# Optimization experiments

Measured on AMD Instinct MI355X. Metric: run time of the kernel, lower is better.

## Reference

```python
import jax, jax.numpy as jnp
import numpy as np

# AF2 IPA dims
N, CS, CZ, E, PQ, PV, H = 768, 384, 128, 16, 4, 8, 12
SCALE_SINGLE = 1.0 / np.sqrt(E)
SCALE_FRAME = -1.0 / np.sqrt(18.0 * PQ)


def setup_inputs() -> dict:
    key = jax.random.key(0)
    ks = jax.random.split(key, 14)
    single = jax.random.normal(ks[0], (N, CS), jnp.float32)
    pair = jax.random.normal(ks[1], (N, N, CZ), jnp.float32)
    R, _ = jnp.linalg.qr(jax.random.normal(ks[2], (N, 3, 3), jnp.float32))  # proper per-residue rotations
    t = jax.random.normal(ks[3], (N, 3), jnp.float32)

    def w(k, shape):
        return jax.random.normal(k, shape, jnp.float32) / np.sqrt(shape[0])

    Wq = w(ks[4], (CS, H * E))
    Wk = w(ks[5], (CS, H * E))
    Wv = w(ks[6], (CS, H * E))
    Wqp = w(ks[7], (CS, H * PQ * 3))
    Wkp = w(ks[8], (CS, H * PQ * 3))
    Wvp = w(ks[9], (CS, H * PV * 3))
    Wb = w(ks[10], (CZ, H))
    D_out = H * (CZ + E + PV * 4)  # 2112
    Wout = w(ks[11], (D_out, CS))
    bout = jnp.zeros((CS,), jnp.float32)
    scale_head = jnp.ones((H,), jnp.float32)
    return dict(single_representation=single, pair_representation=pair,
                frame_rotations=R, frame_translations=t,
                Wq=Wq, Wk=Wk, Wv=Wv, Wqp=Wqp, Wkp=Wkp, Wvp=Wvp,
                Wb=Wb, Wout=Wout, bout=bout, scale_head=scale_head)


def reference(single_representation, pair_representation, frame_rotations, frame_translations,
              Wq, Wk, Wv, Wqp, Wkp, Wvp, Wb, Wout, bout, scale_head):
    s, z, R, t = single_representation, pair_representation, frame_rotations, frame_translations
    # --- attention weights from three sources ---
    q = (s @ Wq).reshape(N, H, E)
    k = (s @ Wk).reshape(N, H, E)
    v = (s @ Wv).reshape(N, H, E)
    w_single = SCALE_SINGLE * jnp.einsum('ihe,jhe->hij', q, k)  # [H,N,N]
    w_pair = (z @ Wb).transpose(2, 0, 1)                        # [H,N,N]

    qp = (s @ Wqp).reshape(N, H, PQ, 3)
    kp = (s @ Wkp).reshape(N, H, PQ, 3)
    # Frame.apply: x_global = R_n x + t_n
    gq = jnp.einsum('nab,nhpb->nhpa', R, qp) + t[:, None, None, :]
    gk = jnp.einsum('nab,nhpb->nhpa', R, kp) + t[:, None, None, :]
    # sum_p ||gq_i^hp - gk_j^hp||^2 expanded to avoid [N,N,H,P,3] intermediate
    sq_q = jnp.sum(gq * gq, axis=(-1, -2)).T   # [H,N]
    sq_k = jnp.sum(gk * gk, axis=(-1, -2)).T   # [H,N]
    dot = jnp.einsum('ihpc,jhpc->hij', gq, gk)
    d2 = sq_q[:, :, None] + sq_k[:, None, :] - 2.0 * dot  # [H,N,N]
    w_frame = SCALE_FRAME * jax.nn.softplus(scale_head)[:, None, None] * d2

    a = jax.nn.softmax(w_single + w_pair + w_frame, axis=-1)  # [H,N,N]

    # --- three value paths ---
    o_s = jnp.einsum('hij,jhe->ihe', a, v).reshape(N, H * E)
    o_z = jnp.einsum('hij,ijc->ihc', a, z).reshape(N, H * CZ)

    vp = (s @ Wvp).reshape(N, H, PV, 3)
    gv = jnp.einsum('nab,nhpb->nhpa', R, vp) + t[:, None, None, :]
    so = jnp.einsum('hij,jhpc->ihpc', a, gv)                    # [N,H,PV,3] in global frame
    # Frame.inverse applied: R_i^T (x - t_i)
    local = jnp.einsum('nba,nhpb->nhpa', R, so - t[:, None, None, :])
    pts = local.transpose(0, 2, 1, 3).reshape(N, PV * H * 3)    # (point, head, xyz) flatten
    norms = jnp.linalg.norm(local, axis=-1).transpose(0, 2, 1).reshape(N, PV * H)

    att = jnp.concatenate([o_s, o_z, pts, norms], axis=-1)      # [N, H*(E+CZ+4*PV)]
    return att @ Wout + bout
```

## Files before the change

### kernel.cpp

```cpp
#include <hip/hip_runtime.h>
#include <hip/hip_bf16.h>

#define NN 768
#define CSD 384
#define CZD 128
#define HD 12
#define DOUT 2112
#define II 2

#define SCALE_SINGLE 0.25f
#define SCALE_FRAME (-0.11785113019775793f)

__device__ __forceinline__ float dot4f(float4 a, float4 b){
    return fmaf(a.x,b.x, fmaf(a.y,b.y, fmaf(a.z,b.z, a.w*b.w)));
}

__global__ __launch_bounds__(384) void k_proj(
    const float* __restrict__ s, const float* __restrict__ R, const float* __restrict__ tv,
    const float* __restrict__ Wq, const float* __restrict__ Wk, const float* __restrict__ Wv,
    const float* __restrict__ Wqp, const float* __restrict__ Wkp, const float* __restrict__ Wvp,
    float* __restrict__ q, float* __restrict__ k, float* __restrict__ v,
    float* __restrict__ gq, float* __restrict__ gk, float* __restrict__ gv,
    float* __restrict__ sqq, float* __restrict__ sqk)
{
    __shared__ float s_l[II*CSD];
    __shared__ float praw[II][576];
    __shared__ float sq_pt[II][96];
    int i0 = blockIdx.x * II, t = threadIdx.x;
    if (t < II*CSD/4){
        const float4* s4 = (const float4*)(s + (size_t)i0*CSD);
        ((float4*)s_l)[t] = s4[t];
    }
    __syncthreads();

    int cols[3] = {t, t+384, t+768};
    const float* Wp[3]; int st[3], lc[3];
    #pragma unroll
    for (int m=0;m<3;m++){
        int c = cols[m];
        if (c < 192){ Wp[m]=Wq;  st[m]=192; lc[m]=c; }
        else if (c < 384){ Wp[m]=Wk;  st[m]=192; lc[m]=c-192; }
        else if (c < 576){ Wp[m]=Wv;  st[m]=192; lc[m]=c-384; }
        else if (c < 720){ Wp[m]=Wqp; st[m]=144; lc[m]=c-576; }
        else if (c < 864){ Wp[m]=Wkp; st[m]=144; lc[m]=c-720; }
        else { Wp[m]=Wvp; st[m]=288; lc[m]=c-864; }
    }
    float acc[3][II];
    #pragma unroll
    for (int m=0;m<3;m++)
        #pragma unroll
        for (int ii=0;ii<II;ii++) acc[m][ii]=0.f;

    #pragma unroll 4
    for (int r=0;r<CSD;r++){
        float w0 = Wp[0][(size_t)r*st[0]+lc[0]];
        float w1 = Wp[1][(size_t)r*st[1]+lc[1]];
        float w2 = Wp[2][(size_t)r*st[2]+lc[2]];
        #pragma unroll
        for (int ii=0;ii<II;ii++){
            float sv = s_l[ii*CSD + r];
            acc[0][ii] = fmaf(sv, w0, acc[0][ii]);
            acc[1][ii] = fmaf(sv, w1, acc[1][ii]);
            acc[2][ii] = fmaf(sv, w2, acc[2][ii]);
        }
    }
    #pragma unroll
    for (int m=0;m<3;m++){
        int c = cols[m];
        #pragma unroll
        for (int ii=0;ii<II;ii++){
            float val = acc[m][ii];
            size_t i = i0 + ii;
            if (c < 192) q[i*192 + c] = val;
            else if (c < 384) k[i*192 + (c-192)] = val;
            else if (c < 576) v[i*192 + (c-384)] = val;
            else praw[ii][c-576] = val;
        }
    }
    __syncthreads();

    if (t < 192){
        #pragma unroll
        for (int ii=0;ii<II;ii++){
            size_t i = i0 + ii;
            const float* Ri = R + i*9;
            float R00=Ri[0],R01=Ri[1],R02=Ri[2];
            float R10=Ri[3],R11=Ri[4],R12=Ri[5];
            float R20=Ri[6],R21=Ri[7],R22=Ri[8];
            float t0=tv[i*3+0],t1=tv[i*3+1],t2=tv[i*3+2];
            int src; float* dst; int sqslot=-1;
            if (t < 48){ src = t*3; dst = gq + i*144 + t*3; sqslot = t; }
            else if (t < 96){ int u=t-48; src = 144+u*3; dst = gk + i*144 + u*3; sqslot = 48+u; }
            else { int u=t-96; src = 288+u*3; dst = gv + i*288 + u*3; }
            float x=praw[ii][src], y=praw[ii][src+1], zc=praw[ii][src+2];
            float g0 = fmaf(R00,x, fmaf(R01,y, fmaf(R02,zc, t0)));
            float g1 = fmaf(R10,x, fmaf(R11,y, fmaf(R12,zc, t1)));
            float g2 = fmaf(R20,x, fmaf(R21,y, fmaf(R22,zc, t2)));
            dst[0]=g0; dst[1]=g1; dst[2]=g2;
            if (sqslot >= 0) sq_pt[ii][sqslot] = g0*g0 + g1*g1 + g2*g2;
        }
    }
    __syncthreads();
    if (t < II*HD){
        int ii = t / HD, h = t % HD;
        float s1 = sq_pt[ii][h*4]+sq_pt[ii][h*4+1]+sq_pt[ii][h*4+2]+sq_pt[ii][h*4+3];
        float s2 = sq_pt[ii][48+h*4]+sq_pt[ii][48+h*4+1]+sq_pt[ii][48+h*4+2]+sq_pt[ii][48+h*4+3];
        sqq[(size_t)(i0+ii)*HD + h] = s1;
        sqk[(size_t)(i0+ii)*HD + h] = s2;
    }
}

__global__ __launch_bounds__(512) void k_ipa(
    const float* __restrict__ z, const float* __restrict__ Wb, const float* __restrict__ scale_head,
    const float* __restrict__ q, const float* __restrict__ k,
    const float* __restrict__ gq, const float* __restrict__ gk,
    const float* __restrict__ sqq, const float* __restrict__ sqk,
    const float* __restrict__ v, const float* __restrict__ gv,
    const float* __restrict__ R, const float* __restrict__ tv,
    float* __restrict__ att)
{
    __shared__ float ztile[2][64][CZD];
    __shared__ float wbT[HD*CZD];
    __shared__ float qloc[360];
    __shared__ float a_l[HD][NN];
    __shared__ float so_l[288];

    int i = blockIdx.x, t = threadIdx.x;
    int wave = t >> 6, lane = t & 63;

    for (int idx=t; idx<HD*CZD; idx+=512){
        int h = idx >> 7, c = idx & 127;
        wbT[idx] = Wb[(size_t)c*HD + h];
    }
    if (t < 192) qloc[t] = q[(size_t)i*192 + t];
    else if (t < 336) qloc[t] = gq[(size_t)i*144 + (t-192)];
    else if (t < 348) qloc[t] = sqq[(size_t)i*HD + (t-336)];
    else if (t < 360){
        int h = t-348;
        float shv = scale_head[h];
        float sp = (shv > 20.f) ? shv : log1pf(__expf(shv));
        qloc[t] = SCALE_FRAME * sp;
    }

    const char* zi = (const char*)(z + (size_t)i*NN*CZD);
    float* zbase = &ztile[0][0][0];

#define STAGEL(JT, BUF) do { \
    const char* _zb = zi + (size_t)(JT)*32768; \
    char* _lb = (char*)zbase + (size_t)(BUF)*32768; \
    _Pragma("unroll") \
    for (int _m=0;_m<4;_m++){ \
        int _d = t*16 + _m*8192; \
        int _j = _d >> 9; \
        int _b = _d & 511; \
        int _sb = _b ^ ((_j & 31) << 4); \
        __builtin_amdgcn_global_load_lds((const __attribute__((address_space(1))) void*)(_zb + (size_t)_j*512 + _sb), \
            (__attribute__((address_space(3))) void*)(_lb + _d), 16, 0, 0); \
    } \
  } while(0)

#define STAGEB(JT, BUF) do { \
    const float* _s = (const float*)zi + (size_t)(JT)*4096 + t*4; \
    float* _d = zbase + (size_t)(BUF)*4096 + t*4; \
    __builtin_amdgcn_global_load_lds((const __attribute__((address_space(1))) void*)_s, \
        (__attribute__((address_space(3))) void*)_d, 16, 0, 0); \
    __builtin_amdgcn_global_load_lds((const __attribute__((address_space(1))) void*)(_s+2048), \
        (__attribute__((address_space(3))) void*)(_d+2048), 16, 0, 0); \
  } while(0)

    STAGEL(0, 0);

    int hg = (wave < 4) ? wave : (wave - 4);
    int h0 = hg * 3;
    float L[12][3];

    __syncthreads();

    {
        const float4* wb4 = (const float4*)wbT;
        const float4* qv4 = (const float4*)qloc;
        const float4* gq4 = (const float4*)(qloc + 192);
        int xoff = (lane & 31) << 4;

        for (int jt=0; jt<12; ++jt){
            int cur = jt & 1;
            if (jt+1 < 12) STAGEL(jt+1, cur^1);
            if (wave < 4){
                const char* zb = (const char*)(zbase + (size_t)cur*8192) + lane*512;
                float p0=0.f, p1=0.f, p2=0.f;
                #pragma unroll 8
                for (int c4=0; c4<32; ++c4){
                    float4 zv = *(const float4*)(zb + ((c4*16) ^ xoff));
                    p0 += dot4f(zv, wb4[(h0+0)*32 + c4]);
                    p1 += dot4f(zv, wb4[(h0+1)*32 + c4]);
                    p2 += dot4f(zv, wb4[(h0+2)*32 + c4]);
                }
                L[jt][0]=p0; L[jt][1]=p1; L[jt][2]=p2;
            } else {
                int jg = jt*64 + lane;
                const float4* kp  = (const float4*)(k  + (size_t)jg*192);
                const float4* gkp = (const float4*)(gk + (size_t)jg*144);
                #pragma unroll
                for (int hs=0; hs<3; ++hs){
                    int h = h0 + hs;
                    float sng = dot4f(qv4[h*4+0], kp[h*4+0]) + dot4f(qv4[h*4+1], kp[h*4+1])
                              + dot4f(qv4[h*4+2], kp[h*4+2]) + dot4f(qv4[h*4+3], kp[h*4+3]);
                    float fdot = dot4f(gq4[h*3+0], gkp[h*3+0]) + dot4f(gq4[h*3+1], gkp[h*3+1])
                               + dot4f(gq4[h*3+2], gkp[h*3+2]);
                    float d2 = qloc[336+h] + sqk[(size_t)jg*HD + h] - 2.0f*fdot;
                    L[jt][hs] = fmaf(SCALE_SINGLE, sng, qloc[348+h]*d2);
                }
            }
            __syncthreads();
        }
    }

    float* S_l = zbase;
    if (wave >= 4){
        int base = (hg*64 + lane) * 37;
        #pragma unroll
        for (int jt=0; jt<12; ++jt)
            #pragma unroll
            for (int hs=0; hs<3; ++hs)
                S_l[base + jt*3 + hs] = L[jt][hs];
    }
    __syncthreads();
    if (wave < 4){
        int base = (hg*64 + lane) * 37;
        #pragma unroll
        for (int jt=0; jt<12; ++jt)
            #pragma unroll
            for (int hs=0; hs<3; ++hs)
                L[jt][hs] += S_l[base + jt*3 + hs];

        #pragma unroll
        for (int hs=0; hs<3; ++hs){
            float m = -1e30f;
            #pragma unroll
            for (int jt=0; jt<12; ++jt) m = fmaxf(m, L[jt][hs]);
            #pragma unroll
            for (int off=32; off; off>>=1) m = fmaxf(m, __shfl_xor(m, off));
            float ssum = 0.f;
            #pragma unroll
            for (int jt=0; jt<12; ++jt){ float e = __expf(L[jt][hs]-m); L[jt][hs]=e; ssum += e; }
            #pragma unroll
            for (int off=32; off; off>>=1) ssum += __shfl_xor(ssum, off);
            float inv = 1.0f/ssum;
            #pragma unroll
            for (int jt=0; jt<12; ++jt){
                a_l[h0+hs][jt*64 + lane] = L[jt][hs]*inv;
            }
        }
    }
    __syncthreads();

    STAGEB(0, 0);

    int hs = 0;
    const float4* gsrc = nullptr;
    int gstride = 0;
    if (t < 384){ hs = t>>5; }
    else if (t < 432){ int u=t-384; hs = u>>2; gsrc = (const float4*)v  + hs*4 + (u&3); gstride = 48; }
    else if (t < 504){ int u=t-432; hs = u/6;  gsrc = (const float4*)gv + hs*6 + (u%6); gstride = 72; }
    float4 acc = {0.f,0.f,0.f,0.f};
    int c4 = t & 31;

    __syncthreads();

    for (int jt=0; jt<24; ++jt){
        int cur = jt & 1;
        if (jt+1 < 24) STAGEB(jt+1, cur^1);
        if (t < 384){
            const float4* arow4 = (const float4*)&a_l[hs][0];
            float4 af[8];
            #pragma unroll
            for (int m=0;m<8;m++) af[m] = arow4[jt*8 + m];
            const float4* zt4 = (const float4*)(zbase + (size_t)cur*4096);
            #pragma unroll
            for (int jj=0;jj<32;jj++){
                float aw = ((const float*)af)[jj];
                float4 zv = zt4[jj*32 + c4];
                acc.x = fmaf(aw, zv.x, acc.x);
                acc.y = fmaf(aw, zv.y, acc.y);
                acc.z = fmaf(aw, zv.z, acc.z);
                acc.w = fmaf(aw, zv.w, acc.w);
            }
        } else if (t < 504){
            const float* arow = &a_l[hs][0];
            #pragma unroll
            for (int jj=0;jj<32;jj++){
                int j = jt*32 + jj;
                float aw = arow[j];
                float4 sv = gsrc[(size_t)j*gstride];
                acc.x = fmaf(aw, sv.x, acc.x);
                acc.y = fmaf(aw, sv.y, acc.y);
                acc.z = fmaf(aw, sv.z, acc.z);
                acc.w = fmaf(aw, sv.w, acc.w);
            }
        }
        __syncthreads();
    }

    if (t < 384){
        float4* dst = (float4*)(att + (size_t)i*DOUT + 192) + (hs*32 + c4);
        *dst = acc;
    } else if (t < 432){
        int u = t-384;
        float4* dst = (float4*)(att + (size_t)i*DOUT) + u;
        *dst = acc;
    } else if (t < 504){
        int u = t-432;
        ((float4*)so_l)[u] = acc;
    }
    __syncthreads();
    if (t < 96){
        int h = t >> 3, p = t & 7;
        float d0 = so_l[h*24+p*3+0] - tv[(size_t)i*3+0];
        float d1 = so_l[h*24+p*3+1] - tv[(size_t)i*3+1];
        float d2 = so_l[h*24+p*3+2] - tv[(size_t)i*3+2];
        const float* Ri = R + (size_t)i*9;
        float l0 = fmaf(Ri[0],d0, fmaf(Ri[3],d1, Ri[6]*d2));
        float l1 = fmaf(Ri[1],d0, fmaf(Ri[4],d1, Ri[7]*d2));
        float l2 = fmaf(Ri[2],d0, fmaf(Ri[5],d1, Ri[8]*d2));
        size_t base = (size_t)i*DOUT;
        att[base + 1728 + p*36 + h*3 + 0] = l0;
        att[base + 1728 + p*36 + h*3 + 1] = l1;
        att[base + 1728 + p*36 + h*3 + 2] = l2;
        att[base + 2016 + p*12 + h] = sqrtf(l0*l0 + l1*l1 + l2*l2);
    }
#undef STAGEL
#undef STAGEB
}

#define ROWS4 2
__global__ __launch_bounds__(384) void k_final(
    const float* __restrict__ att, const float* __restrict__ Wout, const float* __restrict__ bout,
    float* __restrict__ out)
{
    __shared__ float att_l[ROWS4*DOUT];
    int ib = blockIdx.x * ROWS4, t = threadIdx.x;
    for (int idx=t; idx<ROWS4*DOUT; idx+=384){
        att_l[idx] = att[(size_t)ib*DOUT + idx];
    }
    __syncthreads();
    float a0=0.f,a1=0.f,a2=0.f,a3=0.f;
    float b0=0.f,b1=0.f,b2=0.f,b3=0.f;
    #pragma unroll 4
    for (int d=0; d<DOUT; d+=4){
        float w0 = Wout[(size_t)(d+0)*CSD + t];
        float w1 = Wout[(size_t)(d+1)*CSD + t];
        float w2 = Wout[(size_t)(d+2)*CSD + t];
        float w3 = Wout[(size_t)(d+3)*CSD + t];
        a0 = fmaf(att_l[d+0], w0, a0);
        a1 = fmaf(att_l[d+1], w1, a1);
        a2 = fmaf(att_l[d+2], w2, a2);
        a3 = fmaf(att_l[d+3], w3, a3);
        b0 = fmaf(att_l[DOUT+d+0], w0, b0);
        b1 = fmaf(att_l[DOUT+d+1], w1, b1);
        b2 = fmaf(att_l[DOUT+d+2], w2, b2);
        b3 = fmaf(att_l[DOUT+d+3], w3, b3);
    }
    float bb = bout[t];
    out[(size_t)ib*CSD + t]     = bb + ((a0+a1)+(a2+a3));
    out[(size_t)(ib+1)*CSD + t] = bb + ((b0+b1)+(b2+b3));
}

extern "C" void kernel_launch(void* const* d_in, const int* in_sizes, int n_in,
                              void* d_out, int out_size, void* d_ws, size_t ws_size,
                              hipStream_t stream)
{
    const float* s   = (const float*)d_in[0];
    const float* z   = (const float*)d_in[1];
    const float* R   = (const float*)d_in[2];
    const float* tv  = (const float*)d_in[3];
    const float* Wq  = (const float*)d_in[4];
    const float* Wk  = (const float*)d_in[5];
    const float* Wv  = (const float*)d_in[6];
    const float* Wqp = (const float*)d_in[7];
    const float* Wkp = (const float*)d_in[8];
    const float* Wvp = (const float*)d_in[9];
    const float* Wb  = (const float*)d_in[10];
    const float* Wout= (const float*)d_in[11];
    const float* bout= (const float*)d_in[12];
    const float* sh  = (const float*)d_in[13];

    float* ws  = (float*)d_ws;
    float* q_  = ws;
    float* k_  = q_  + 147456;
    float* v_  = k_  + 147456;
    float* gq_ = v_  + 147456;
    float* gk_ = gq_ + 110592;
    float* gv_ = gk_ + 110592;
    float* sqq_= gv_ + 221184;
    float* sqk_= sqq_ + 9216;
    float* att_= sqk_ + 9216;
    float* out = (float*)d_out;

    hipLaunchKernelGGL(k_proj,  dim3(NN/II), dim3(384), 0, stream,
                       s,R,tv,Wq,Wk,Wv,Wqp,Wkp,Wvp, q_,k_,v_,gq_,gk_,gv_,sqq_,sqk_);
    hipLaunchKernelGGL(k_ipa,   dim3(NN),    dim3(512), 0, stream,
                       z,Wb,sh,q_,k_,gq_,gk_,sqq_,sqk_, v_,gv_,R,tv, att_);
    hipLaunchKernelGGL(k_final, dim3(NN/ROWS4), dim3(384), 0, stream,
                       att_,Wout,bout, out);
}
```

Before: 435.7 us.

## Split pair-bias dot product across lanes with register-resident Wb and shuffle reduction

In the pair-bias phase, each lane now handles a quarter of the channel dimension for four rows instead of all 128 channels for one row. The Wb slices for its three heads stay in registers, and partial sums are combined with cross-lane shuffles. This removes repeated LDS reads of Wb and changes the LDS access pattern on the z tile. It also adds launch_bounds min-blocks 2, which adds register pressure from the wbr array against that occupancy cap, and it remaps row indices (jj) for the merge and softmax.

```diff
diff --git a/kernel.cpp b/kernel.cpp
--- a/kernel.cpp
+++ b/kernel.cpp
@@ -110,7 +110,7 @@
     }
 }
 
-__global__ __launch_bounds__(512) void k_ipa(
+__global__ __launch_bounds__(512, 2) void k_ipa(
     const float* __restrict__ z, const float* __restrict__ Wb, const float* __restrict__ scale_head,
     const float* __restrict__ q, const float* __restrict__ k,
     const float* __restrict__ gq, const float* __restrict__ gk,
@@ -174,28 +174,62 @@
     int h0 = hg * 3;
     float L[12][3];
 
-    __syncthreads();
+    int qq = lane >> 4, jl = lane & 15;
+    int jj = jl*4 + qq;
+
+    __syncthreads();
+
+    float4 wbr[3][8];
+    if (wave < 4){
+        const float4* wb4 = (const float4*)wbT;
+        #pragma unroll
+        for (int hs=0; hs<3; ++hs)
+            #pragma unroll
+            for (int cc=0; cc<8; ++cc)
+                wbr[hs][cc] = wb4[(h0+hs)*32 + cc*4 + qq];
+    }
 
     {
-        const float4* wb4 = (const float4*)wbT;
         const float4* qv4 = (const float4*)qloc;
         const float4* gq4 = (const float4*)(qloc + 192);
-        int xoff = (lane & 31) << 4;
 
         for (int jt=0; jt<12; ++jt){
             int cur = jt & 1;
             if (jt+1 < 12) STAGEL(jt+1, cur^1);
             if (wave < 4){
-                const char* zb = (const char*)(zbase + (size_t)cur*8192) + lane*512;
-                float p0=0.f, p1=0.f, p2=0.f;
-                #pragma unroll 8
-                for (int c4=0; c4<32; ++c4){
-                    float4 zv = *(const float4*)(zb + ((c4*16) ^ xoff));
-                    p0 += dot4f(zv, wb4[(h0+0)*32 + c4]);
-                    p1 += dot4f(zv, wb4[(h0+1)*32 + c4]);
-                    p2 += dot4f(zv, wb4[(h0+2)*32 + c4]);
+                const char* zb = (const char*)(zbase + (size_t)cur*8192);
+                float p[4][3];
+                #pragma unroll
+                for (int r=0;r<4;r++)
+                    #pragma unroll
+                    for (int hs=0;hs<3;hs++) p[r][hs]=0.f;
+                #pragma unroll
+                for (int r=0; r<4; ++r){
+                    int row = jl*4 + r;
+                    const char* zr = zb + (size_t)row*512;
+                    int xo = (row & 31) << 4;
+                    #pragma unroll
+                    for (int cc=0; cc<8; ++cc){
+                        float4 zv = *(const float4*)(zr + ((16*(cc*4+qq)) ^ xo));
+                        p[r][0] += dot4f(zv, wbr[0][cc]);
+                        p[r][1] += dot4f(zv, wbr[1][cc]);
+                        p[r][2] += dot4f(zv, wbr[2][cc]);
+                    }
                 }
-                L[jt][0]=p0; L[jt][1]=p1; L[jt][2]=p2;
+                #pragma unroll
+                for (int r=0; r<4; ++r)
+                    #pragma unroll
+                    for (int hs=0; hs<3; ++hs){
+                        float vv = p[r][hs];
+                        vv += __shfl_xor(vv, 16);
+                        vv += __shfl_xor(vv, 32);
+                        p[r][hs] = vv;
+                    }
+                #pragma unroll
+                for (int hs=0; hs<3; ++hs){
+                    float vv = (qq==0) ? p[0][hs] : (qq==1) ? p[1][hs] : (qq==2) ? p[2][hs] : p[3][hs];
+                    L[jt][hs] = vv;
+                }
             } else {
                 int jg = jt*64 + lane;
                 const float4* kp  = (const float4*)(k  + (size_t)jg*192);
@@ -226,7 +260,7 @@
     }
     __syncthreads();
     if (wave < 4){
-        int base = (hg*64 + lane) * 37;
+        int base = (hg*64 + jj) * 37;
         #pragma unroll
         for (int jt=0; jt<12; ++jt)
             #pragma unroll
@@ -248,7 +282,7 @@
             float inv = 1.0f/ssum;
             #pragma unroll
             for (int jt=0; jt<12; ++jt){
-                a_l[h0+hs][jt*64 + lane] = L[jt][hs]*inv;
+                a_l[h0+hs][jt*64 + jj] = L[jt][hs]*inv;
             }
         }
     }
@@ -277,9 +311,9 @@
             for (int m=0;m<8;m++) af[m] = arow4[jt*8 + m];
             const float4* zt4 = (const float4*)(zbase + (size_t)cur*4096);
             #pragma unroll
-            for (int jj=0;jj<32;jj++){
-                float aw = ((const float*)af)[jj];
-                float4 zv = zt4[jj*32 + c4];
+            for (int jj2=0;jj2<32;jj2++){
+                float aw = ((const float*)af)[jj2];
+                float4 zv = zt4[jj2*32 + c4];
                 acc.x = fmaf(aw, zv.x, acc.x);
                 acc.y = fmaf(aw, zv.y, acc.y);
                 acc.z = fmaf(aw, zv.z, acc.z);
@@ -288,8 +322,8 @@
         } else if (t < 504){
             const float* arow = &a_l[hs][0];
             #pragma unroll
-            for (int jj=0;jj<32;jj++){
-                int j = jt*32 + jj;
+            for (int jj2=0;jj2<32;jj2++){
+                int j = jt*32 + jj2;
                 float aw = arow[j];
                 float4 sv = gsrc[(size_t)j*gstride];
                 acc.x = fmaf(aw, sv.x, acc.x);
```

New measurement: 456.1 us. 4.7% more time.

## Register-block two heads per wave and stage larger pair tiles in the value pass

Applied to the files above, without the earlier changes.

The pair-value accumulation now has each wave compute two heads at once. Each z element loaded from LDS feeds two FMA chains, and the two lane halves split the j range and are combined with a cross-lane shuffle at the end. Staged z tiles double from 32 to 64 rows, so the loop runs 12 iterations instead of 24 and needs half as many barriers. This cuts LDS reads per FMA and synchronisation overhead, at the cost of more registers and a larger double buffer, which the earlier ztile allocation must already fit.

```diff
diff --git a/kernel.cpp b/kernel.cpp
--- a/kernel.cpp
+++ b/kernel.cpp
@@ -160,12 +160,14 @@
   } while(0)
 
 #define STAGEB(JT, BUF) do { \
-    const float* _s = (const float*)zi + (size_t)(JT)*4096 + t*4; \
-    float* _d = zbase + (size_t)(BUF)*4096 + t*4; \
-    __builtin_amdgcn_global_load_lds((const __attribute__((address_space(1))) void*)_s, \
-        (__attribute__((address_space(3))) void*)_d, 16, 0, 0); \
-    __builtin_amdgcn_global_load_lds((const __attribute__((address_space(1))) void*)(_s+2048), \
-        (__attribute__((address_space(3))) void*)(_d+2048), 16, 0, 0); \
+    const char* _zb = zi + (size_t)(JT)*32768; \
+    char* _lb = (char*)zbase + (size_t)(BUF)*32768; \
+    _Pragma("unroll") \
+    for (int _m=0;_m<4;_m++){ \
+        int _d = t*16 + _m*8192; \
+        __builtin_amdgcn_global_load_lds((const __attribute__((address_space(1))) void*)(_zb + _d), \
+            (__attribute__((address_space(3))) void*)(_lb + _d), 16, 0, 0); \
+    } \
   } while(0)
 
     STAGEL(0, 0);
@@ -256,61 +258,71 @@
 
     STAGEB(0, 0);
 
-    int hs = 0;
-    const float4* gsrc = nullptr;
-    int gstride = 0;
-    if (t < 384){ hs = t>>5; }
-    else if (t < 432){ int u=t-384; hs = u>>2; gsrc = (const float4*)v  + hs*4 + (u&3); gstride = 48; }
-    else if (t < 504){ int u=t-432; hs = u/6;  gsrc = (const float4*)gv + hs*6 + (u%6); gstride = 72; }
-    float4 acc = {0.f,0.f,0.f,0.f};
-    int c4 = t & 31;
-
-    __syncthreads();
-
-    for (int jt=0; jt<24; ++jt){
+    int c4 = lane & 31, jhalf = lane >> 5;
+    int h0b = wave*2;
+    float4 azA = {0,0,0,0}, azB = {0,0,0,0};
+    float4 accs = {0,0,0,0};
+    const float4* gsrc = nullptr; int gstride = 0; int hso = 0;
+    if (t >= 384 && t < 432){ int u=t-384; hso = u>>2; gsrc = (const float4*)v  + hso*4 + (u&3); gstride = 48; }
+    else if (t >= 432 && t < 504){ int u=t-432; hso = u/6;  gsrc = (const float4*)gv + hso*6 + (u%6); gstride = 72; }
+
+    __syncthreads();
+
+    for (int jt=0; jt<12; ++jt){
         int cur = jt & 1;
-        if (jt+1 < 24) STAGEB(jt+1, cur^1);
+        if (jt+1 < 12) STAGEB(jt+1, cur^1);
         if (t < 384){
-            const float4* arow4 = (const float4*)&a_l[hs][0];
-            float4 af[8];
-            #pragma unroll
-            for (int m=0;m<8;m++) af[m] = arow4[jt*8 + m];
-            const float4* zt4 = (const float4*)(zbase + (size_t)cur*4096);
+            const float4* aA = (const float4*)&a_l[h0b  ][0] + jt*16 + jhalf*8;
+            const float4* aB = (const float4*)&a_l[h0b+1][0] + jt*16 + jhalf*8;
+            float4 afA[8], afB[8];
+            #pragma unroll
+            for (int m=0;m<8;m++){ afA[m]=aA[m]; afB[m]=aB[m]; }
+            const float4* zt4 = (const float4*)(zbase + (size_t)cur*8192) + (size_t)jhalf*1024;
             #pragma unroll
             for (int jj=0;jj<32;jj++){
-                float aw = ((const float*)af)[jj];
                 float4 zv = zt4[jj*32 + c4];
-                acc.x = fmaf(aw, zv.x, acc.x);
-                acc.y = fmaf(aw, zv.y, acc.y);
-                acc.z = fmaf(aw, zv.z, acc.z);
-                acc.w = fmaf(aw, zv.w, acc.w);
+                float wa = ((const float*)afA)[jj];
+                float wb = ((const float*)afB)[jj];
+                azA.x = fmaf(wa, zv.x, azA.x);
+                azA.y = fmaf(wa, zv.y, azA.y);
+                azA.z = fmaf(wa, zv.z, azA.z);
+                azA.w = fmaf(wa, zv.w, azA.w);
+                azB.x = fmaf(wb, zv.x, azB.x);
+                azB.y = fmaf(wb, zv.y, azB.y);
+                azB.z = fmaf(wb, zv.z, azB.z);
+                azB.w = fmaf(wb, zv.w, azB.w);
             }
         } else if (t < 504){
-            const float* arow = &a_l[hs][0];
-            #pragma unroll
-            for (int jj=0;jj<32;jj++){
-                int j = jt*32 + jj;
+            const float* arow = &a_l[hso][0];
+            #pragma unroll
+            for (int jj=0;jj<64;jj++){
+                int j = jt*64 + jj;
                 float aw = arow[j];
                 float4 sv = gsrc[(size_t)j*gstride];
-                acc.x = fmaf(aw, sv.x, acc.x);
-                acc.y = fmaf(aw, sv.y, acc.y);
-                acc.z = fmaf(aw, sv.z, acc.z);
-                acc.w = fmaf(aw, sv.w, acc.w);
+                accs.x = fmaf(aw, sv.x, accs.x);
+                accs.y = fmaf(aw, sv.y, accs.y);
+                accs.z = fmaf(aw, sv.z, accs.z);
+                accs.w = fmaf(aw, sv.w, accs.w);
             }
         }
         __syncthreads();
     }
 
     if (t < 384){
-        float4* dst = (float4*)(att + (size_t)i*DOUT + 192) + (hs*32 + c4);
-        *dst = acc;
+        azA.x += __shfl_xor(azA.x, 32); azA.y += __shfl_xor(azA.y, 32);
+        azA.z += __shfl_xor(azA.z, 32); azA.w += __shfl_xor(azA.w, 32);
+        azB.x += __shfl_xor(azB.x, 32); azB.y += __shfl_xor(azB.y, 32);
+        azB.z += __shfl_xor(azB.z, 32); azB.w += __shfl_xor(azB.w, 32);
+        if (jhalf == 0){
+            *(float4*)(att + (size_t)i*DOUT + 192 + (h0b  )*128 + c4*4) = azA;
+            *(float4*)(att + (size_t)i*DOUT + 192 + (h0b+1)*128 + c4*4) = azB;
+        }
     } else if (t < 432){
         int u = t-384;
-        float4* dst = (float4*)(att + (size_t)i*DOUT) + u;
-        *dst = acc;
+        ((float4*)(att + (size_t)i*DOUT))[u] = accs;
     } else if (t < 504){
         int u = t-432;
-        ((float4*)so_l)[u] = acc;
+        ((float4*)so_l)[u] = accs;
     }
     __syncthreads();
     if (t < 96){
```

New measurement: 436.9 us. Within noise of the previous version (+0.3%).
